# Kernel tuning notes

Hardware: AMD Instinct MI355X
Metric: run time of the kernel (lower is better)

The kernel has to match this reference:

```python
import jax, jax.numpy as jnp
import numpy as np

TY = 10  # decoder loop uses the global Ty=10 in the original code


def _bi_lstm_dir(X, Wih, Whh, b, n_hidden):
    # X: (m, T, F); returns hidden states (m, T, n_hidden). Gate order: i,f,g,o.
    m = X.shape[0]
    def step(carry, x_t):
        h, c = carry
        g = x_t @ Wih.T + h @ Whh.T + b
        i, f, gg, o = jnp.split(g, 4, axis=-1)
        c = jax.nn.sigmoid(f) * c + jax.nn.sigmoid(i) * jnp.tanh(gg)
        h = jax.nn.sigmoid(o) * jnp.tanh(c)
        return (h, c), h
    h0 = jnp.zeros((m, n_hidden), X.dtype)
    _, hs = jax.lax.scan(step, (h0, h0), jnp.swapaxes(X, 0, 1))
    return jnp.swapaxes(hs, 0, 1)


def setup_inputs() -> dict:
    key = jax.random.key(0)
    ks = jax.random.split(key, 17)
    m, Tx, F = 256, 256, 128
    n_a, n_s, vocab, attn_h = 256, 512, 1024, 10
    def w(k, shape, fan_in):
        return (jax.random.normal(k, shape, jnp.float32) / np.sqrt(fan_in)).astype(jnp.float32)
    return {
        "X": jax.random.normal(ks[0], (m, Tx, F), jnp.float32),
        "Wih_f": w(ks[1], (4 * n_a, F), F),
        "Whh_f": w(ks[2], (4 * n_a, n_a), n_a),
        "b_f": w(ks[3], (4 * n_a,), n_a),
        "Wih_b": w(ks[4], (4 * n_a, F), F),
        "Whh_b": w(ks[5], (4 * n_a, n_a), n_a),
        "b_b": w(ks[6], (4 * n_a,), n_a),
        "W1": w(ks[7], (attn_h, 2 * n_a + n_s), 2 * n_a + n_s),
        "b1": w(ks[8], (attn_h,), attn_h),
        "W2": w(ks[9], (1, attn_h), attn_h),
        "b2": w(ks[10], (1,), attn_h),
        "Wc_ih": w(ks[11], (4 * n_s, n_s), n_s),
        "Wc_hh": w(ks[12], (4 * n_s, n_s), n_s),
        "bc": w(ks[13], (4 * n_s,), n_s),
        "Wfc": w(ks[14], (vocab, n_s), n_s),
        "bfc": w(ks[15], (vocab,), n_s),
    }


def reference(X, Wih_f, Whh_f, b_f, Wih_b, Whh_b, b_b, W1, b1, W2, b2, Wc_ih, Wc_hh, bc, Wfc, bfc):
    m, Tx, _ = X.shape
    n_a = Whh_f.shape[1]
    n_s = Wc_hh.shape[1]
    # bidirectional encoder
    a_f = _bi_lstm_dir(X, Wih_f, Whh_f, b_f, n_a)
    a_b = _bi_lstm_dir(X[:, ::-1], Wih_b, Whh_b, b_b, n_a)[:, ::-1]
    a = jnp.concatenate([a_f, a_b], axis=-1)  # (m, Tx, 2*n_a)
    # decoder: initial h_n = zeros(m, 2, n_a).flatten(1) == zeros(m, n_s) since n_s = 2*n_a
    s = jnp.zeros((m, n_s), X.dtype)
    c = jnp.zeros((m, n_s), X.dtype)
    outs = []
    for _ in range(TY):
        sp = jnp.broadcast_to(s[:, None, :], (m, Tx, n_s))
        concat = jnp.concatenate([a, sp], axis=-1)           # (m, Tx, 2*n_a + n_s)
        e = jnp.tanh(concat @ W1.T + b1)                     # (m, Tx, 10)
        scores = jax.nn.relu(e @ W2.T + b2)                  # (m, Tx, 1)
        alphas = jax.nn.softmax(scores, axis=1)              # softmax over Tx
        context = jnp.sum(alphas * a, axis=1)                # (m, 2*n_a) == (m, n_s)
        g = context @ Wc_ih.T + s @ Wc_hh.T + bc             # LSTMCell
        i, f, gg, o = jnp.split(g, 4, axis=-1)
        c = jax.nn.sigmoid(f) * c + jax.nn.sigmoid(i) * jnp.tanh(gg)
        s = jax.nn.sigmoid(o) * jnp.tanh(c)
        outs.append(s @ Wfc.T + bfc)                         # (m, vocab)
    return jnp.stack(outs, axis=1)                           # (m, Ty, vocab)
```

## Files before the change

### kernel.cpp

```cpp
#include <hip/hip_runtime.h>
#include <hip/hip_bf16.h>

#define TXN 256
#define NA 256
#define NF 128
#define NS 512
#define TYN 10
#define VOCAB 1024

#define A_STR 392
#define W_STR 392
#define WL_OFF (64 * W_STR)
#define AH_OFF (2 * 64 * W_STR)
#define AL_OFF (AH_OFF + 32 * A_STR)
#define PRE_OFF_US (AL_OFF + 32 * A_STR)
#define ENC_LDS_BYTES (150528 + 32 * 68 * 4 + 64 * 4)

#define D_STR 264
#define D_WH 0
#define D_WL (64 * D_STR)
#define D_AH (2 * 64 * D_STR)
#define D_AL (D_AH + 32 * D_STR)
#define D_PRE_US (D_AL + 32 * D_STR)
#define DEC_LDS_BYTES (101376 + 32 * 68 * 4 + 64 * 4)

typedef __attribute__((ext_vector_type(8))) short bf16x8;
typedef __attribute__((ext_vector_type(4))) float f32x4;

__device__ __forceinline__ float fsigmoid(float x) { return 1.f / (1.f + __expf(-x)); }
__device__ __forceinline__ float ftanh(float x)    { return 1.f - 2.f / (1.f + __expf(2.f * x)); }

__device__ __forceinline__ void split_bf16(float v, unsigned short& hi, unsigned short& lo) {
    __hip_bfloat16 h = __float2bfloat16(v);
    float rem = v - __bfloat162float(h);
    __hip_bfloat16 l = __float2bfloat16(rem);
    hi = *reinterpret_cast<unsigned short*>(&h);
    lo = *reinterpret_cast<unsigned short*>(&l);
}

__device__ __forceinline__ float agent_ld(const float* p) {
    return __hip_atomic_load(p, __ATOMIC_RELAXED, __HIP_MEMORY_SCOPE_AGENT);
}
__device__ __forceinline__ void agent_st(float* p, float v) {
    __hip_atomic_store(p, v, __ATOMIC_RELAXED, __HIP_MEMORY_SCOPE_AGENT);
}
__device__ __forceinline__ unsigned flag_ld(const unsigned* p) {
    return __hip_atomic_load(p, __ATOMIC_RELAXED, __HIP_MEMORY_SCOPE_AGENT);
}
__device__ __forceinline__ void flag_st(unsigned* p, unsigned v) {
    __hip_atomic_store(p, v, __ATOMIC_RELAXED, __HIP_MEMORY_SCOPE_AGENT);
}

__global__ __launch_bounds__(512, 1) void encoder_kernel(
    const float* __restrict__ X,
    const float* __restrict__ Wih_f, const float* __restrict__ Whh_f, const float* __restrict__ b_f,
    const float* __restrict__ Wih_b, const float* __restrict__ Whh_b, const float* __restrict__ b_b,
    float* __restrict__ a, unsigned int* __restrict__ bar)
{
    extern __shared__ unsigned char smem_raw[];
    unsigned short* Wh  = (unsigned short*)smem_raw;
    unsigned short* Wl  = (unsigned short*)smem_raw + WL_OFF;
    unsigned short* Ahh = (unsigned short*)smem_raw + AH_OFF;
    unsigned short* All = (unsigned short*)smem_raw + AL_OFF;
    float* Pre = (float*)(smem_raw + (size_t)PRE_OFF_US * 2);
    float* bsh = Pre + 32 * 68;

    const int tid = threadIdx.x;
    const int dir = blockIdx.x & 1;
    const int bid = blockIdx.x >> 1;
    const int i0 = (bid >> 4) * 32;
    const int j0 = (bid & 15) * 16;
    const int grp = dir * 8 + (bid >> 4);
    const int myjb = bid & 15;
    unsigned int* slots = bar + grp * 16;

    const float* __restrict__ Wih = dir ? Wih_b : Wih_f;
    const float* __restrict__ Whh = dir ? Whh_b : Whh_f;
    const float* __restrict__ bv  = dir ? b_b  : b_f;

    if (tid < 64) bsh[tid] = bv[(tid >> 4) * NA + j0 + (tid & 15)];

    {
        const int col = tid & 255;
        const int r0w = (tid >> 8) * 32;
        for (int r = r0w; r < r0w + 32; ++r) {
            int row = (r >> 4) * NA + j0 + (r & 15);
            unsigned short hi, lo;
            split_bf16(Whh[(size_t)row * NA + col], hi, lo);
            Wh[r * W_STR + col] = hi;
            Wl[r * W_STR + col] = lo;
            if (col < NF) {
                split_bf16(Wih[(size_t)row * NF + col], hi, lo);
                Wh[r * W_STR + 256 + col] = hi;
                Wl[r * W_STR + 256 + col] = lo;
            }
        }
    }

    {
        const int col = tid & 255;
        const int r0z = (tid >> 8) * 16;
        #pragma unroll 4
        for (int r = r0z; r < r0z + 16; ++r) {
            Ahh[r * A_STR + col] = 0;
            All[r * A_STR + col] = 0;
        }
    }

    {
        const int t0 = dir ? (TXN - 1) : 0;
        const int kx = tid & 127;
        const int rbase = tid >> 7;
        #pragma unroll 4
        for (int rr = 0; rr < 8; ++rr) {
            int r = rr * 4 + rbase;
            float v = X[((size_t)(i0 + r) * TXN + t0) * NF + kx];
            unsigned short hi, lo;
            split_bf16(v, hi, lo);
            Ahh[r * A_STR + 256 + kx] = hi;
            All[r * A_STR + 256 + kx] = lo;
        }
    }

    float cC = 0.f;
    const int jl  = tid & 15;
    const int epr = tid >> 4;

    const int lane = tid & 63;
    const int wv   = tid >> 6;
    const int rt   = wv >> 1;
    const int g0   = (wv & 1) * 2;
    const int ln   = lane & 15;
    const int quad = lane >> 4;
    const unsigned short* pAh = Ahh + (rt * 16 + ln) * A_STR + quad * 8;
    const unsigned short* pAl = All + (rt * 16 + ln) * A_STR + quad * 8;
    const unsigned short* pW0h = Wh + (g0 * 16 + ln) * W_STR + quad * 8;
    const unsigned short* pW0l = Wl + (g0 * 16 + ln) * W_STR + quad * 8;
    const unsigned short* pW1h = pW0h + 16 * W_STR;
    const unsigned short* pW1l = pW0l + 16 * W_STR;

    for (int step = 0; step < TXN; ++step) {
        const int t = dir ? (TXN - 1 - step) : step;

        if (step != 0) {
            const int tprev = dir ? (t + 1) : (t - 1);
            const int colh = tid & 255;
            const int r0h = (tid >> 8) * 16;
            const int jw = colh >> 4;
            while (flag_ld(&slots[jw]) < (unsigned)step) {}
            float hv[16];
            #pragma unroll
            for (int r = 0; r < 16; ++r) {
                hv[r] = agent_ld(&a[(((size_t)(i0 + r0h + r) * TXN + tprev) << 9) + dir * NA + colh]);
            }
            #pragma unroll
            for (int r = 0; r < 16; ++r) {
                unsigned short hi, lo;
                split_bf16(hv[r], hi, lo);
                Ahh[(r0h + r) * A_STR + colh] = hi;
                All[(r0h + r) * A_STR + colh] = lo;
            }
        }
        __syncthreads();

        if (tid < 256) {
            f32x4 a0e = {0.f,0.f,0.f,0.f}, a0o = {0.f,0.f,0.f,0.f};
            f32x4 a1e = {0.f,0.f,0.f,0.f}, a1o = {0.f,0.f,0.f,0.f};
            #pragma unroll
            for (int kp = 0; kp < 6; ++kp) {
                {
                    const int kc = kp * 2;
                    bf16x8 fah = *(const bf16x8*)(pAh + kc * 32);
                    bf16x8 fal = *(const bf16x8*)(pAl + kc * 32);
                    bf16x8 w0h = *(const bf16x8*)(pW0h + kc * 32);
                    bf16x8 w0l = *(const bf16x8*)(pW0l + kc * 32);
                    bf16x8 w1h = *(const bf16x8*)(pW1h + kc * 32);
                    bf16x8 w1l = *(const bf16x8*)(pW1l + kc * 32);
                    a0e = __builtin_amdgcn_mfma_f32_16x16x32_bf16(fal, w0h, a0e, 0, 0, 0);
                    a0e = __builtin_amdgcn_mfma_f32_16x16x32_bf16(fah, w0l, a0e, 0, 0, 0);
                    a0e = __builtin_amdgcn_mfma_f32_16x16x32_bf16(fah, w0h, a0e, 0, 0, 0);
                    a1e = __builtin_amdgcn_mfma_f32_16x16x32_bf16(fal, w1h, a1e, 0, 0, 0);
                    a1e = __builtin_amdgcn_mfma_f32_16x16x32_bf16(fah, w1l, a1e, 0, 0, 0);
                    a1e = __builtin_amdgcn_mfma_f32_16x16x32_bf16(fah, w1h, a1e, 0, 0, 0);
                }
                {
                    const int kc = kp * 2 + 1;
                    bf16x8 fah = *(const bf16x8*)(pAh + kc * 32);
                    bf16x8 fal = *(const bf16x8*)(pAl + kc * 32);
                    bf16x8 w0h = *(const bf16x8*)(pW0h + kc * 32);
                    bf16x8 w0l = *(const bf16x8*)(pW0l + kc * 32);
                    bf16x8 w1h = *(const bf16x8*)(pW1h + kc * 32);
                    bf16x8 w1l = *(const bf16x8*)(pW1l + kc * 32);
                    a0o = __builtin_amdgcn_mfma_f32_16x16x32_bf16(fal, w0h, a0o, 0, 0, 0);
                    a0o = __builtin_amdgcn_mfma_f32_16x16x32_bf16(fah, w0l, a0o, 0, 0, 0);
                    a0o = __builtin_amdgcn_mfma_f32_16x16x32_bf16(fah, w0h, a0o, 0, 0, 0);
                    a1o = __builtin_amdgcn_mfma_f32_16x16x32_bf16(fal, w1h, a1o, 0, 0, 0);
                    a1o = __builtin_amdgcn_mfma_f32_16x16x32_bf16(fah, w1l, a1o, 0, 0, 0);
                    a1o = __builtin_amdgcn_mfma_f32_16x16x32_bf16(fah, w1h, a1o, 0, 0, 0);
                }
            }
            #pragma unroll
            for (int reg = 0; reg < 4; ++reg) {
                int prow = rt * 16 + quad * 4 + reg;
                Pre[prow * 68 + g0 * 16 + ln]       = a0e[reg] + a0o[reg];
                Pre[prow * 68 + (g0 + 1) * 16 + ln] = a1e[reg] + a1o[reg];
            }
        }
        __syncthreads();

        {
            float gi = fsigmoid(Pre[epr * 68 +      jl] + bsh[jl]);
            float gf = fsigmoid(Pre[epr * 68 + 16 + jl] + bsh[16 + jl]);
            float gg = ftanh  (Pre[epr * 68 + 32 + jl] + bsh[32 + jl]);
            float go = fsigmoid(Pre[epr * 68 + 48 + jl] + bsh[48 + jl]);
            cC = gf * cC + gi * gg;
            float h = go * ftanh(cC);
            agent_st(&a[(((size_t)(i0 + epr) * TXN + t) << 9) + dir * NA + j0 + jl], h);
        }

        if (step != TXN - 1) {
            __syncthreads();
            if (tid == 0) flag_st(&slots[myjb], (unsigned)(step + 1));
            {
                const int tn = dir ? (t - 1) : (t + 1);
                const int kx = tid & 127;
                const int rbase = tid >> 7;
                #pragma unroll 4
                for (int rr = 0; rr < 8; ++rr) {
                    int r = rr * 4 + rbase;
                    float v = X[((size_t)(i0 + r) * TXN + tn) * NF + kx];
                    unsigned short hi, lo;
                    split_bf16(v, hi, lo);
                    Ahh[r * A_STR + 256 + kx] = hi;
                    All[r * A_STR + 256 + kx] = lo;
                }
            }
        }
    }
}

__global__ __launch_bounds__(256) void wsplit_cat(
    const float* __restrict__ Wc_ih, const float* __restrict__ Wc_hh,
    unsigned short* __restrict__ Wh, unsigned short* __restrict__ Wl)
{
    int idx = blockIdx.x * 256 + threadIdx.x;
    int r = idx >> 10, k = idx & 1023;
    float v = (k < 512) ? Wc_ih[(size_t)r * 512 + k] : Wc_hh[(size_t)r * 512 + (k - 512)];
    unsigned short hi, lo;
    split_bf16(v, hi, lo);
    Wh[idx] = hi; Wl[idx] = lo;
}

__global__ __launch_bounds__(256) void wsplit_fc(
    const float* __restrict__ Wfc,
    unsigned short* __restrict__ Wh, unsigned short* __restrict__ Wl)
{
    int idx = blockIdx.x * 256 + threadIdx.x;
    unsigned short hi, lo;
    split_bf16(Wfc[idx], hi, lo);
    Wh[idx] = hi; Wl[idx] = lo;
}

__global__ __launch_bounds__(256) void attn_prep(
    const float* __restrict__ a, const float* __restrict__ W1,
    const float* __restrict__ b1, float* __restrict__ aW1)
{
    __shared__ float Wsh[10][516];
    __shared__ float red[64][10][4];
    const int tid = threadIdx.x;
    for (int idx = tid; idx < 10 * 512; idx += 256) {
        int o = idx >> 9, k = idx & 511;
        Wsh[o][k] = W1[o * 1024 + k];
    }
    __syncthreads();
    const int r = tid >> 2, kq = tid & 3;
    const float* ar = a + ((size_t)blockIdx.x * 64 + r) * 512 + kq * 128;
    float acc[10] = {};
    for (int k = 0; k < 128; k += 4) {
        float4 v = *(const float4*)&ar[k];
        #pragma unroll
        for (int o = 0; o < 10; ++o) {
            float4 w = *(const float4*)&Wsh[o][kq * 128 + k];
            acc[o] += v.x * w.x + v.y * w.y + v.z * w.z + v.w * w.w;
        }
    }
    #pragma unroll
    for (int o = 0; o < 10; ++o) red[r][o][kq] = acc[o];
    __syncthreads();
    for (int idx = tid; idx < 640; idx += 256) {
        int rr = idx / 10, o = idx % 10;
        float s = red[rr][o][0] + red[rr][o][1] + red[rr][o][2] + red[rr][o][3] + b1[o];
        aW1[((size_t)blockIdx.x * 64 + rr) * 10 + o] = s;
    }
}

__global__ __launch_bounds__(256) void attn_kernel(
    const float* __restrict__ aW1,
    const float* __restrict__ s_prev, int sp_stride,
    const float* __restrict__ W1,
    const float* __restrict__ W2,
    const float* __restrict__ b2,
    const float* __restrict__ a,
    float* __restrict__ xcat)
{
    __shared__ float sh_s[10];
    __shared__ float sh_w2[10];
    __shared__ float sred[160];
    __shared__ float red[256];
    __shared__ float al[256];
    __shared__ float4 ctxred[256];
    const int i = blockIdx.x;
    const int tid = threadIdx.x;

    if (tid < 160) {
        int o = tid >> 4, part = tid & 15;
        const float* srow = s_prev + (size_t)i * sp_stride;
        const float* wrow = W1 + o * 1024 + 512;
        float p = 0.f;
        for (int k = part; k < 512; k += 16) p += srow[k] * wrow[k];
        sred[tid] = p;
    }
    __syncthreads();
    if (tid < 10) {
        float v = 0.f;
        #pragma unroll
        for (int p = 0; p < 16; ++p) v += sred[tid * 16 + p];
        sh_s[tid] = v;
        sh_w2[tid] = W2[tid];
    }
    __syncthreads();

    float sum = b2[0];
    const float* ar = aW1 + ((size_t)i * TXN + tid) * 10;
    #pragma unroll
    for (int h = 0; h < 10; ++h) {
        float e = ftanh(ar[h] + sh_s[h]);
        sum += e * sh_w2[h];
    }
    float sc = fmaxf(sum, 0.f);

    red[tid] = sc;
    __syncthreads();
    for (int s = 128; s > 0; s >>= 1) {
        if (tid < s) red[tid] = fmaxf(red[tid], red[tid + s]);
        __syncthreads();
    }
    float mx = red[0];
    __syncthreads();
    float p = __expf(sc - mx);
    red[tid] = p;
    __syncthreads();
    for (int s = 128; s > 0; s >>= 1) {
        if (tid < s) red[tid] += red[tid + s];
        __syncthreads();
    }
    float inv = 1.f / red[0];
    al[tid] = p * inv;
    __syncthreads();

    const int half = tid >> 7;
    const int q    = tid & 127;
    const float* abase = a + (size_t)i * TXN * NS + q * 4;
    float4 acc = make_float4(0.f, 0.f, 0.f, 0.f);
    #pragma unroll 8
    for (int t = half; t < TXN; t += 2) {
        float w = al[t];
        float4 v = *(const float4*)&abase[(size_t)t * NS];
        acc.x += w * v.x; acc.y += w * v.y; acc.z += w * v.z; acc.w += w * v.w;
    }
    ctxred[tid] = acc;
    __syncthreads();
    if (tid < 128) {
        float4 e = ctxred[tid];
        float4 o = ctxred[tid + 128];
        float4 r4 = make_float4(e.x + o.x, e.y + o.y, e.z + o.z, e.w + o.w);
        *(float4*)&xcat[(size_t)i * 512 + tid * 4] = r4;
    }
}

__global__ __launch_bounds__(256, 1) void gates_kernel(
    const float* __restrict__ xcat,
    const float* __restrict__ s_prev, int sp_stride,
    const unsigned short* __restrict__ Wch,
    const unsigned short* __restrict__ Wcl,
    const float* __restrict__ bc,
    float* __restrict__ c_buf,
    float* __restrict__ s_out, int so_stride)
{
    extern __shared__ unsigned char smem_raw[];
    unsigned short* Wh = (unsigned short*)smem_raw + D_WH;
    unsigned short* Wl = (unsigned short*)smem_raw + D_WL;
    unsigned short* Ah = (unsigned short*)smem_raw + D_AH;
    unsigned short* Al = (unsigned short*)smem_raw + D_AL;
    float* Pre = (float*)(smem_raw + (size_t)D_PRE_US * 2);
    float* bsh = Pre + 32 * 68;

    const int tid = threadIdx.x;
    const int i0 = blockIdx.x * 32;
    const int j0 = blockIdx.y * 16;

    if (tid < 64) bsh[tid] = bc[(tid >> 4) * 512 + j0 + (tid & 15)];

    const int lane = tid & 63;
    const int wv   = tid >> 6;
    const int rt   = wv >> 1;
    const int g0   = (wv & 1) * 2;
    const int ln   = lane & 15;
    const int quad = lane >> 4;
    const unsigned short* pAh = Ah + (rt * 16 + ln) * D_STR + quad * 8;
    const unsigned short* pAl = Al + (rt * 16 + ln) * D_STR + quad * 8;
    const unsigned short* pW0h = Wh + (g0 * 16 + ln) * D_STR + quad * 8;
    const unsigned short* pW0l = Wl + (g0 * 16 + ln) * D_STR + quad * 8;
    const unsigned short* pW1h = pW0h + 16 * D_STR;
    const unsigned short* pW1l = pW0l + 16 * D_STR;

    const int rW = tid >> 2;
    const int qW = (tid & 3) * 64;
    const int rowg = (rW >> 4) * 512 + j0 + (rW & 15);

    f32x4 a0 = {0.f,0.f,0.f,0.f}, a1 = {0.f,0.f,0.f,0.f};

    for (int ch = 0; ch < 4; ++ch) {
        const int kc0 = ch * 256;
        __syncthreads();
        #pragma unroll 8
        for (int r = 0; r < 32; ++r) {
            float v;
            if (ch < 2) v = xcat[(size_t)(i0 + r) * 512 + kc0 + tid];
            else        v = s_prev[(size_t)(i0 + r) * sp_stride + (kc0 - 512) + tid];
            unsigned short hi, lo;
            split_bf16(v, hi, lo);
            Ah[r * D_STR + tid] = hi;
            Al[r * D_STR + tid] = lo;
        }
        {
            const size_t base = (size_t)rowg * 1024 + kc0 + qW;
            #pragma unroll
            for (int i = 0; i < 8; ++i) {
                *(bf16x8*)&Wh[rW * D_STR + qW + i * 8] = *(const bf16x8*)&Wch[base + i * 8];
                *(bf16x8*)&Wl[rW * D_STR + qW + i * 8] = *(const bf16x8*)&Wcl[base + i * 8];
            }
        }
        __syncthreads();
        #pragma unroll
        for (int kc = 0; kc < 8; ++kc) {
            bf16x8 fah = *(const bf16x8*)(pAh + kc * 32);
            bf16x8 fal = *(const bf16x8*)(pAl + kc * 32);
            bf16x8 w0h = *(const bf16x8*)(pW0h + kc * 32);
            bf16x8 w0l = *(const bf16x8*)(pW0l + kc * 32);
            bf16x8 w1h = *(const bf16x8*)(pW1h + kc * 32);
            bf16x8 w1l = *(const bf16x8*)(pW1l + kc * 32);
            a0 = __builtin_amdgcn_mfma_f32_16x16x32_bf16(fal, w0h, a0, 0, 0, 0);
            a0 = __builtin_amdgcn_mfma_f32_16x16x32_bf16(fah, w0l, a0, 0, 0, 0);
            a0 = __builtin_amdgcn_mfma_f32_16x16x32_bf16(fah, w0h, a0, 0, 0, 0);
            a1 = __builtin_amdgcn_mfma_f32_16x16x32_bf16(fal, w1h, a1, 0, 0, 0);
            a1 = __builtin_amdgcn_mfma_f32_16x16x32_bf16(fah, w1l, a1, 0, 0, 0);
            a1 = __builtin_amdgcn_mfma_f32_16x16x32_bf16(fah, w1h, a1, 0, 0, 0);
        }
    }
    __syncthreads();
    #pragma unroll
    for (int reg = 0; reg < 4; ++reg) {
        int prow = rt * 16 + quad * 4 + reg;
        Pre[prow * 68 + g0 * 16 + ln]       = a0[reg];
        Pre[prow * 68 + (g0 + 1) * 16 + ln] = a1[reg];
    }
    __syncthreads();

    const int jl = tid & 15;
    const int iA = (tid >> 4) * 2;
    #pragma unroll
    for (int rr = 0; rr < 2; ++rr) {
        int r = iA + rr;
        float gi = fsigmoid(Pre[r * 68 +      jl] + bsh[jl]);
        float gf = fsigmoid(Pre[r * 68 + 16 + jl] + bsh[16 + jl]);
        float gg = ftanh  (Pre[r * 68 + 32 + jl] + bsh[32 + jl]);
        float go = fsigmoid(Pre[r * 68 + 48 + jl] + bsh[48 + jl]);
        size_t ci = (size_t)(i0 + r) * 512 + j0 + jl;
        float cn = gf * c_buf[ci] + gi * gg;
        c_buf[ci] = cn;
        s_out[(size_t)(i0 + r) * so_stride + j0 + jl] = go * ftanh(cn);
    }
}

__global__ __launch_bounds__(256, 1) void logits_kernel(
    const float* __restrict__ S, int s_stride,
    const unsigned short* __restrict__ Wfh,
    const unsigned short* __restrict__ Wfl,
    const float* __restrict__ bfc,
    float* __restrict__ out, int o_stride, int o_off)
{
    extern __shared__ unsigned char smem_raw[];
    unsigned short* Wh = (unsigned short*)smem_raw + D_WH;
    unsigned short* Wl = (unsigned short*)smem_raw + D_WL;
    unsigned short* Ah = (unsigned short*)smem_raw + D_AH;
    unsigned short* Al = (unsigned short*)smem_raw + D_AL;

    const int tid = threadIdx.x;
    const int i0 = blockIdx.x * 32;
    const int v0 = blockIdx.y * 64;

    const int lane = tid & 63;
    const int wv   = tid >> 6;
    const int rt   = wv >> 1;
    const int ct   = wv & 1;
    const int ln   = lane & 15;
    const int quad = lane >> 4;
    const unsigned short* pAh = Ah + (rt * 16 + ln) * D_STR + quad * 8;
    const unsigned short* pAl = Al + (rt * 16 + ln) * D_STR + quad * 8;
    const unsigned short* pW0h = Wh + (ct * 32 + ln) * D_STR + quad * 8;
    const unsigned short* pW0l = Wl + (ct * 32 + ln) * D_STR + quad * 8;
    const unsigned short* pW1h = pW0h + 16 * D_STR;
    const unsigned short* pW1l = pW0l + 16 * D_STR;

    const int rW = tid >> 2;
    const int qW = (tid & 3) * 64;

    f32x4 a0 = {0.f,0.f,0.f,0.f}, a1 = {0.f,0.f,0.f,0.f};

    for (int ch = 0; ch < 2; ++ch) {
        const int kc0 = ch * 256;
        __syncthreads();
        #pragma unroll 8
        for (int r = 0; r < 32; ++r) {
            float v = S[(size_t)(i0 + r) * s_stride + kc0 + tid];
            unsigned short hi, lo;
            split_bf16(v, hi, lo);
            Ah[r * D_STR + tid] = hi;
            Al[r * D_STR + tid] = lo;
        }
        {
            const size_t base = (size_t)(v0 + rW) * 512 + kc0 + qW;
            #pragma unroll
            for (int i = 0; i < 8; ++i) {
                *(bf16x8*)&Wh[rW * D_STR + qW + i * 8] = *(const bf16x8*)&Wfh[base + i * 8];
                *(bf16x8*)&Wl[rW * D_STR + qW + i * 8] = *(const bf16x8*)&Wfl[base + i * 8];
            }
        }
        __syncthreads();
        #pragma unroll
        for (int kc = 0; kc < 8; ++kc) {
            bf16x8 fah = *(const bf16x8*)(pAh + kc * 32);
            bf16x8 fal = *(const bf16x8*)(pAl + kc * 32);
            bf16x8 w0h = *(const bf16x8*)(pW0h + kc * 32);
            bf16x8 w0l = *(const bf16x8*)(pW0l + kc * 32);
            bf16x8 w1h = *(const bf16x8*)(pW1h + kc * 32);
            bf16x8 w1l = *(const bf16x8*)(pW1l + kc * 32);
            a0 = __builtin_amdgcn_mfma_f32_16x16x32_bf16(fal, w0h, a0, 0, 0, 0);
            a0 = __builtin_amdgcn_mfma_f32_16x16x32_bf16(fah, w0l, a0, 0, 0, 0);
            a0 = __builtin_amdgcn_mfma_f32_16x16x32_bf16(fah, w0h, a0, 0, 0, 0);
            a1 = __builtin_amdgcn_mfma_f32_16x16x32_bf16(fal, w1h, a1, 0, 0, 0);
            a1 = __builtin_amdgcn_mfma_f32_16x16x32_bf16(fah, w1l, a1, 0, 0, 0);
            a1 = __builtin_amdgcn_mfma_f32_16x16x32_bf16(fah, w1h, a1, 0, 0, 0);
        }
    }
    #pragma unroll
    for (int reg = 0; reg < 4; ++reg) {
        int row = i0 + rt * 16 + quad * 4 + reg;
        int col0 = v0 + ct * 32 + ln;
        out[(size_t)row * o_stride + o_off + col0]      = a0[reg] + bfc[col0];
        out[(size_t)row * o_stride + o_off + col0 + 16] = a1[reg] + bfc[col0 + 16];
    }
}

extern "C" void kernel_launch(void* const* d_in, const int* in_sizes, int n_in,
                              void* d_out, int out_size, void* d_ws, size_t ws_size,
                              hipStream_t stream)
{
    const float* X     = (const float*)d_in[0];
    const float* Wih_f = (const float*)d_in[1];
    const float* Whh_f = (const float*)d_in[2];
    const float* b_f   = (const float*)d_in[3];
    const float* Wih_b = (const float*)d_in[4];
    const float* Whh_b = (const float*)d_in[5];
    const float* b_b   = (const float*)d_in[6];
    const float* W1    = (const float*)d_in[7];
    const float* b1    = (const float*)d_in[8];
    const float* W2    = (const float*)d_in[9];
    const float* b2    = (const float*)d_in[10];
    const float* Wc_ih = (const float*)d_in[11];
    const float* Wc_hh = (const float*)d_in[12];
    const float* bc    = (const float*)d_in[13];
    const float* Wfc   = (const float*)d_in[14];
    const float* bfc   = (const float*)d_in[15];
    float* out = (float*)d_out;
    float* ws  = (float*)d_ws;

    float* c_buf = ws;
    float* zbuf  = ws + 131072;
    float* sbufB = ws + 262144;
    float* xcat  = ws + 393216;
    float* a     = ws + 524288;
    float* aW1   = ws + 34078720;
    unsigned short* Wch = (unsigned short*)(ws + 34734080);
    unsigned short* Wcl = (unsigned short*)(ws + 35782656);
    unsigned short* Wfh = (unsigned short*)(ws + 36831232);
    unsigned short* Wfl = (unsigned short*)(ws + 37093376);
    unsigned int* bar   = (unsigned int*)(ws + 37355520);
    float* S_all = ws + 37355776;
    const int deferred = (ws_size >= (size_t)38666496 * sizeof(float)) ? 1 : 0;

    static int attrs_set = 0;
    if (!attrs_set) {
        hipFuncSetAttribute(reinterpret_cast<const void*>(encoder_kernel),
                            hipFuncAttributeMaxDynamicSharedMemorySize, ENC_LDS_BYTES);
        hipFuncSetAttribute(reinterpret_cast<const void*>(gates_kernel),
                            hipFuncAttributeMaxDynamicSharedMemorySize, DEC_LDS_BYTES);
        hipFuncSetAttribute(reinterpret_cast<const void*>(logits_kernel),
                            hipFuncAttributeMaxDynamicSharedMemorySize, DEC_LDS_BYTES);
        attrs_set = 1;
    }

    hipMemsetAsync(c_buf, 0, (size_t)262144 * sizeof(float), stream);
    hipMemsetAsync(bar, 0, 256 * sizeof(unsigned int), stream);

    wsplit_cat<<<8192, 256, 0, stream>>>(Wc_ih, Wc_hh, Wch, Wcl);
    wsplit_fc<<<2048, 256, 0, stream>>>(Wfc, Wfh, Wfl);

    {
        void* args[] = { (void*)&X, (void*)&Wih_f, (void*)&Whh_f, (void*)&b_f,
                         (void*)&Wih_b, (void*)&Whh_b, (void*)&b_b, (void*)&a, (void*)&bar };
        hipLaunchCooperativeKernel(reinterpret_cast<void*>(encoder_kernel),
                                   dim3(256), dim3(512), args, ENC_LDS_BYTES, stream);
    }

    attn_prep<<<1024, 256, 0, stream>>>(a, W1, b1, aW1);

    for (int ty = 0; ty < TYN; ++ty) {
        const float* sprev; int spstr;
        float* sout; int sostr;
        if (ty == 0) { sprev = zbuf; spstr = 512; }
        else if (deferred) { sprev = S_all + (size_t)(ty - 1) * 512; spstr = TYN * 512; }
        else { sprev = (ty & 1) ? sbufB : zbuf; spstr = 512; }
        if (deferred) { sout = S_all + (size_t)ty * 512; sostr = TYN * 512; }
        else { sout = (ty & 1) ? zbuf : sbufB; sostr = 512; }

        attn_kernel<<<256, 256, 0, stream>>>(aW1, sprev, spstr, W1, W2, b2, a, xcat);
        gates_kernel<<<dim3(8, 32), 256, DEC_LDS_BYTES, stream>>>(
            xcat, sprev, spstr, Wch, Wcl, bc, c_buf, sout, sostr);
        if (!deferred) {
            logits_kernel<<<dim3(8, 16), 256, DEC_LDS_BYTES, stream>>>(
                sout, 512, Wfh, Wfl, bfc, out, TYN * VOCAB, ty * VOCAB);
        }
    }
    if (deferred) {
        logits_kernel<<<dim3(80, 16), 256, DEC_LDS_BYTES, stream>>>(
            S_all, 512, Wfh, Wfl, bfc, out, VOCAB, 0);
    }
}
```

Measured before the change: 2.013 ms.

## Overlap input-projection MFMAs with h exchange and remap blocks to XCDs

Block indices are remapped so that all blocks of one batch group land on the same XCD, which keeps the cross-block h exchange within one L2. Within each step, waves 0-3 now compute the X-part of the gate matmul (k-chunks 8-11) before the barrier. Meanwhile waves 4-7 wait on the flags and load the previous h for all 32 rows. This hides the recurrent-dependency latency behind independent work. An extra barrier is added after the X prefetch to keep the next step's early MFMA reads correct.

```diff
diff --git a/kernel.cpp b/kernel.cpp
--- a/kernel.cpp
+++ b/kernel.cpp
@@ -66,12 +66,15 @@
     float* bsh = Pre + 32 * 68;
 
     const int tid = threadIdx.x;
-    const int dir = blockIdx.x & 1;
-    const int bid = blockIdx.x >> 1;
-    const int i0 = (bid >> 4) * 32;
-    const int j0 = (bid & 15) * 16;
-    const int grp = dir * 8 + (bid >> 4);
-    const int myjb = bid & 15;
+    const int xcd = blockIdx.x & 7;
+    const int sub = (blockIdx.x >> 3) & 1;
+    const int jb  = blockIdx.x >> 4;
+    const int dir = sub;
+    const int ig  = xcd;
+    const int i0 = ig * 32;
+    const int j0 = jb * 16;
+    const int grp = dir * 8 + ig;
+    const int myjb = jb;
     unsigned int* slots = bar + grp * 16;
 
     const float* __restrict__ Wih = dir ? Wih_b : Wih_f;
@@ -121,6 +124,7 @@
             All[r * A_STR + 256 + kx] = lo;
         }
     }
+    __syncthreads();
 
     float cC = 0.f;
     const int jl  = tid & 15;
@@ -142,32 +146,58 @@
     for (int step = 0; step < TXN; ++step) {
         const int t = dir ? (TXN - 1 - step) : step;
 
-        if (step != 0) {
+        f32x4 a0e = {0.f,0.f,0.f,0.f}, a0o = {0.f,0.f,0.f,0.f};
+        f32x4 a1e = {0.f,0.f,0.f,0.f}, a1o = {0.f,0.f,0.f,0.f};
+
+        if (tid < 256) {
+            #pragma unroll
+            for (int k4 = 0; k4 < 4; ++k4) {
+                const int kc = 8 + k4;
+                bf16x8 fah = *(const bf16x8*)(pAh + kc * 32);
+                bf16x8 fal = *(const bf16x8*)(pAl + kc * 32);
+                bf16x8 w0h = *(const bf16x8*)(pW0h + kc * 32);
+                bf16x8 w0l = *(const bf16x8*)(pW0l + kc * 32);
+                bf16x8 w1h = *(const bf16x8*)(pW1h + kc * 32);
+                bf16x8 w1l = *(const bf16x8*)(pW1l + kc * 32);
+                if ((kc & 1) == 0) {
+                    a0e = __builtin_amdgcn_mfma_f32_16x16x32_bf16(fal, w0h, a0e, 0, 0, 0);
+                    a0e = __builtin_amdgcn_mfma_f32_16x16x32_bf16(fah, w0l, a0e, 0, 0, 0);
+                    a0e = __builtin_amdgcn_mfma_f32_16x16x32_bf16(fah, w0h, a0e, 0, 0, 0);
+                    a1e = __builtin_amdgcn_mfma_f32_16x16x32_bf16(fal, w1h, a1e, 0, 0, 0);
+                    a1e = __builtin_amdgcn_mfma_f32_16x16x32_bf16(fah, w1l, a1e, 0, 0, 0);
+                    a1e = __builtin_amdgcn_mfma_f32_16x16x32_bf16(fah, w1h, a1e, 0, 0, 0);
+                } else {
+                    a0o = __builtin_amdgcn_mfma_f32_16x16x32_bf16(fal, w0h, a0o, 0, 0, 0);
+                    a0o = __builtin_amdgcn_mfma_f32_16x16x32_bf16(fah, w0l, a0o, 0, 0, 0);
+                    a0o = __builtin_amdgcn_mfma_f32_16x16x32_bf16(fah, w0h, a0o, 0, 0, 0);
+                    a1o = __builtin_amdgcn_mfma_f32_16x16x32_bf16(fal, w1h, a1o, 0, 0, 0);
+                    a1o = __builtin_amdgcn_mfma_f32_16x16x32_bf16(fah, w1l, a1o, 0, 0, 0);
+                    a1o = __builtin_amdgcn_mfma_f32_16x16x32_bf16(fah, w1h, a1o, 0, 0, 0);
+                }
+            }
+        } else if (step != 0) {
             const int tprev = dir ? (t + 1) : (t - 1);
             const int colh = tid & 255;
-            const int r0h = (tid >> 8) * 16;
             const int jw = colh >> 4;
             while (flag_ld(&slots[jw]) < (unsigned)step) {}
-            float hv[16];
+            float hv[32];
             #pragma unroll
-            for (int r = 0; r < 16; ++r) {
-                hv[r] = agent_ld(&a[(((size_t)(i0 + r0h + r) * TXN + tprev) << 9) + dir * NA + colh]);
+            for (int r = 0; r < 32; ++r) {
+                hv[r] = agent_ld(&a[(((size_t)(i0 + r) * TXN + tprev) << 9) + dir * NA + colh]);
             }
             #pragma unroll
-            for (int r = 0; r < 16; ++r) {
+            for (int r = 0; r < 32; ++r) {
                 unsigned short hi, lo;
                 split_bf16(hv[r], hi, lo);
-                Ahh[(r0h + r) * A_STR + colh] = hi;
-                All[(r0h + r) * A_STR + colh] = lo;
+                Ahh[r * A_STR + colh] = hi;
+                All[r * A_STR + colh] = lo;
             }
         }
         __syncthreads();
 
         if (tid < 256) {
-            f32x4 a0e = {0.f,0.f,0.f,0.f}, a0o = {0.f,0.f,0.f,0.f};
-            f32x4 a1e = {0.f,0.f,0.f,0.f}, a1o = {0.f,0.f,0.f,0.f};
             #pragma unroll
-            for (int kp = 0; kp < 6; ++kp) {
+            for (int kp = 0; kp < 4; ++kp) {
                 {
                     const int kc = kp * 2;
                     bf16x8 fah = *(const bf16x8*)(pAh + kc * 32);
@@ -235,6 +265,7 @@
                     All[r * A_STR + 256 + kx] = lo;
                 }
             }
+            __syncthreads();
         }
     }
 }
```

Result: faster. 1.936 ms (-3.8%).
